# Kernel optimization log

Hardware: AMD Instinct MI355X
Metric: run time of the kernel (lower is better)

Reference implementation:

```python
import jax, jax.numpy as jnp
import numpy as np


def setup_inputs() -> dict:
    key = jax.random.key(0)
    ks = jax.random.split(key, 8)
    H = 4096
    T = 2048
    s = 0.02  # keep gates out of saturation
    return {
        "start_tensor": jax.random.normal(ks[0], (400,), jnp.float32),
        "encoder_hidden": jax.random.normal(ks[1], (1, 1, H), jnp.float32) * 0.1,
        "W_ih": jax.random.normal(ks[2], (3 * H, 400), jnp.float32) * s,
        "W_hh": jax.random.normal(ks[3], (3 * H, H), jnp.float32) * s,
        "b_ih": jax.random.normal(ks[4], (3 * H,), jnp.float32) * s,
        "b_hh": jax.random.normal(ks[5], (3 * H,), jnp.float32) * s,
        "W_out": jax.random.normal(ks[6], (401, H), jnp.float32) * s,
        "b_out": jax.random.normal(ks[7], (401,), jnp.float32) * s,
        "max_length": 2048,
    }


def reference(start_tensor, encoder_hidden, W_ih, W_hh, b_ih, b_hh, W_out, b_out, max_length):
    H = W_hh.shape[1]
    # The original loop feeds relu(start_tensor) as input at EVERY step
    # (input is never reassigned), so the input-side gate pre-activations
    # are loop-invariant and can be precomputed.
    x = jax.nn.relu(start_tensor)                      # [400]
    gx = W_ih @ x + b_ih                               # [3H]
    gx_r, gx_z, gx_n = gx[:H], gx[H:2 * H], gx[2 * H:]

    def step(h, _):
        gh = W_hh @ h + b_hh                           # [3H]
        r = jax.nn.sigmoid(gx_r + gh[:H])
        z = jax.nn.sigmoid(gx_z + gh[H:2 * H])
        n = jnp.tanh(gx_n + r * gh[2 * H:])
        h_new = (1.0 - z) * n + z * h                  # PyTorch GRU update
        o = W_out @ h_new + b_out                      # [401]
        out = jnp.tanh(o[:400])                        # [400]
        stop = jax.nn.sigmoid(o[400:])                 # [1]
        return h_new, (out, stop)

    h0 = encoder_hidden.reshape(H)
    _, (outputs, stops) = jax.lax.scan(step, h0, None, length=max_length)
    # outputs: [T, 400], stops: [T, 1]. The torch code breaks early when
    # stop > 0.5 (data-dependent length); here we run all steps (jit-safe).
    return outputs, stops
```

## Files before the change

### kernel.cpp

```cpp
#include <hip/hip_runtime.h>
#include <math.h>

#define NBLOCKS 256
#define NTHREADS 512
#define WPB 8
#define HDIM 4096
#define NPAIR (HDIM/2)

typedef _Float16 f16x2  __attribute__((ext_vector_type(2)));
typedef _Float16 f16x16 __attribute__((ext_vector_type(16)));
typedef unsigned long long u64;

union UF { unsigned u; f16x2 h; };

__device__ __forceinline__ float dot2f(f16x2 a, f16x2 b, float c) {
  return __builtin_amdgcn_fdot2(a, b, c, false);
}
__device__ __forceinline__ float sigmoidf_(float x) {
  return 1.0f / (1.0f + __expf(-x));
}
__device__ __forceinline__ float tanhf_(float x) {
  float a = fabsf(x);
  float t = __expf(-2.0f * a);
  float r = (1.0f - t) / (1.0f + t);
  return copysignf(r, x);
}
__device__ __forceinline__ void st64(u64* p, u64 v) {
  __hip_atomic_store(p, v, __ATOMIC_RELAXED, __HIP_MEMORY_SCOPE_AGENT);
}
__device__ __forceinline__ u64 ld64(const u64* p) {
  return __hip_atomic_load(p, __ATOMIC_RELAXED, __HIP_MEMORY_SCOPE_AGENT);
}

#define LOAD_CHUNK(VAR, SRC, C) do {                                          \
  const float2* s_ = (const float2*)(SRC) + lane + 64 * ((C) * 8);            \
  float2 p0_ = s_[0];   float2 p1_ = s_[64];  float2 p2_ = s_[128];           \
  float2 p3_ = s_[192]; float2 p4_ = s_[256]; float2 p5_ = s_[320];           \
  float2 p6_ = s_[384]; float2 p7_ = s_[448];                                 \
  VAR = (f16x16){ (_Float16)p0_.x, (_Float16)p0_.y, (_Float16)p1_.x, (_Float16)p1_.y, \
                  (_Float16)p2_.x, (_Float16)p2_.y, (_Float16)p3_.x, (_Float16)p3_.y, \
                  (_Float16)p4_.x, (_Float16)p4_.y, (_Float16)p5_.x, (_Float16)p5_.y, \
                  (_Float16)p6_.x, (_Float16)p6_.y, (_Float16)p7_.x, (_Float16)p7_.y }; \
} while (0)

#define LOAD_ROW(K, GATE, IDX) do {                                           \
  const float* sr_ = W_hh + ((size_t)(GATE) * HDIM + (i0 + (IDX))) * HDIM;    \
  LOAD_CHUNK(w##K##_0, sr_, 0); LOAD_CHUNK(w##K##_1, sr_, 1);                 \
  LOAD_CHUNK(w##K##_2, sr_, 2); LOAD_CHUNK(w##K##_3, sr_, 3);                 \
} while (0)

#define PAIR(V, J) (__builtin_shufflevector((V), (V), 2 * (J), 2 * (J) + 1))

#define DOT8(K, C)                                                            \
  a##K = dot2f(PAIR(w##K##_##C, 0), hp0, a##K);                               \
  a##K = dot2f(PAIR(w##K##_##C, 1), hp1, a##K);                               \
  a##K = dot2f(PAIR(w##K##_##C, 2), hp2, a##K);                               \
  a##K = dot2f(PAIR(w##K##_##C, 3), hp3, a##K);                               \
  a##K = dot2f(PAIR(w##K##_##C, 4), hp4, a##K);                               \
  a##K = dot2f(PAIR(w##K##_##C, 5), hp5, a##K);                               \
  a##K = dot2f(PAIR(w##K##_##C, 6), hp6, a##K);                               \
  a##K = dot2f(PAIR(w##K##_##C, 7), hp7, a##K);

#define CHUNK_STEP(C) {                                                       \
  UF u0_, u1_, u2_, u3_, u4_, u5_, u6_, u7_;                                  \
  u0_.u = h_lds[lane + 64 * ((C) * 8 + 0)];                                   \
  u1_.u = h_lds[lane + 64 * ((C) * 8 + 1)];                                   \
  u2_.u = h_lds[lane + 64 * ((C) * 8 + 2)];                                   \
  u3_.u = h_lds[lane + 64 * ((C) * 8 + 3)];                                   \
  u4_.u = h_lds[lane + 64 * ((C) * 8 + 4)];                                   \
  u5_.u = h_lds[lane + 64 * ((C) * 8 + 5)];                                   \
  u6_.u = h_lds[lane + 64 * ((C) * 8 + 6)];                                   \
  u7_.u = h_lds[lane + 64 * ((C) * 8 + 7)];                                   \
  f16x2 hp0 = u0_.h, hp1 = u1_.h, hp2 = u2_.h, hp3 = u3_.h;                   \
  f16x2 hp4 = u4_.h, hp5 = u5_.h, hp6 = u6_.h, hp7 = u7_.h;                   \
  DOT8(0, C) DOT8(1, C) DOT8(2, C) DOT8(3, C) DOT8(4, C) DOT8(5, C)          \
}

#define GX_INIT(K, GATE, IDX) {                                               \
  const int row_ = (GATE) * HDIM + (i0 + (IDX));                              \
  const float* s_ = W_ih + (size_t)row_ * 400;                                \
  float acc_ = 0.0f;                                                          \
  for (int c = lane; c < 400; c += 64) acc_ += s_[c] * x_lds[c];              \
  _Pragma("unroll")                                                           \
  for (int o = 32; o; o >>= 1) acc_ += __shfl_xor(acc_, o, 64);               \
  acc_ += b_ih[row_];                                                         \
  if ((GATE) != 2) acc_ += b_hh[row_];                                        \
  gx##K = acc_;                                                               \
}

__global__ __attribute__((amdgpu_flat_work_group_size(NTHREADS, NTHREADS),
                          amdgpu_waves_per_eu(2, 2)))
void gru_persistent(const float* __restrict__ start,
                    const float* __restrict__ enc_h,
                    const float* __restrict__ W_ih,
                    const float* __restrict__ W_hh,
                    const float* __restrict__ b_ih,
                    const float* __restrict__ b_hh,
                    const float* __restrict__ W_out,
                    const float* __restrict__ b_out,
                    float* __restrict__ out,
                    u64* __restrict__ ws,
                    int T)
{
  __shared__ unsigned h_lds[NPAIR];
  __shared__ unsigned wout_lds[2][NPAIR];
  __shared__ float    x_lds[400];

  const int tid  = threadIdx.x;
  const int b    = blockIdx.x;
  const int wave = tid >> 6;
  const int lane = tid & 63;
  const int g    = b * WPB + wave;
  const int i0   = 2 * g;

  u64* buf0 = ws;
  u64* buf1 = ws + NPAIR;

  if (tid < 400) x_lds[tid] = fmaxf(start[tid], 0.0f);
  for (int s = 0; s < 2; ++s) {
    int row = 2 * b + s;
    if (row < 401) {
      for (int p = tid; p < NPAIR; p += NTHREADS) {
        float2 wv = *(const float2*)(W_out + (size_t)row * HDIM + 2 * p);
        UF u; u.h = (f16x2){(_Float16)wv.x, (_Float16)wv.y};
        wout_lds[s][p] = u.u;
      }
    }
  }
  __syncthreads();

  f16x16 w0_0, w0_1, w0_2, w0_3;
  f16x16 w1_0, w1_1, w1_2, w1_3;
  f16x16 w2_0, w2_1, w2_2, w2_3;
  f16x16 w3_0, w3_1, w3_2, w3_3;
  f16x16 w4_0, w4_1, w4_2, w4_3;
  f16x16 w5_0, w5_1, w5_2, w5_3;
  LOAD_ROW(0, 0, 0); LOAD_ROW(1, 0, 1);
  LOAD_ROW(2, 1, 0); LOAD_ROW(3, 1, 1);
  LOAD_ROW(4, 2, 0); LOAD_ROW(5, 2, 1);

  float gx0, gx1, gx2, gx3, gx4, gx5;
  GX_INIT(0, 0, 0); GX_INIT(1, 0, 1);
  GX_INIT(2, 1, 0); GX_INIT(3, 1, 1);
  GX_INIT(4, 2, 0); GX_INIT(5, 2, 1);
  const float bhn0 = b_hh[2 * HDIM + i0];
  const float bhn1 = b_hh[2 * HDIM + i0 + 1];

  float h0 = enc_h[i0], h1 = enc_h[i0 + 1];

  if (lane == 0) {
    UF u; u.h = (f16x2){(_Float16)h0, (_Float16)h1};
    st64(&buf0[g], ((u64)1 << 32) | (u64)u.u);
  }

  for (int t = 0; t < T; ++t) {
    u64* rd = (t & 1) ? buf1 : buf0;
    u64* wr = (t & 1) ? buf0 : buf1;
    const unsigned exp = (unsigned)(t + 1);

    {
      const int p0 = tid, p1 = tid + NTHREADS, p2 = tid + 2 * NTHREADS, p3 = tid + 3 * NTHREADS;
      u64 v0, v1, v2, v3;
      for (;;) {
        v0 = ld64(rd + p0); v1 = ld64(rd + p1);
        v2 = ld64(rd + p2); v3 = ld64(rd + p3);
        if ((unsigned)(v0 >> 32) == exp && (unsigned)(v1 >> 32) == exp &&
            (unsigned)(v2 >> 32) == exp && (unsigned)(v3 >> 32) == exp) break;
        __builtin_amdgcn_s_sleep(1);
      }
      h_lds[p0] = (unsigned)v0; h_lds[p1] = (unsigned)v1;
      h_lds[p2] = (unsigned)v2; h_lds[p3] = (unsigned)v3;
    }
    __syncthreads();

    float a0 = 0.f, a1 = 0.f, a2 = 0.f, a3 = 0.f, a4 = 0.f, a5 = 0.f;
    CHUNK_STEP(0); CHUNK_STEP(1); CHUNK_STEP(2); CHUNK_STEP(3);
    #pragma unroll
    for (int off = 32; off; off >>= 1) {
      a0 += __shfl_xor(a0, off, 64);
      a1 += __shfl_xor(a1, off, 64);
      a2 += __shfl_xor(a2, off, 64);
      a3 += __shfl_xor(a3, off, 64);
      a4 += __shfl_xor(a4, off, 64);
      a5 += __shfl_xor(a5, off, 64);
    }

    float r0 = sigmoidf_(gx0 + a0);
    float r1 = sigmoidf_(gx1 + a1);
    float z0 = sigmoidf_(gx2 + a2);
    float z1 = sigmoidf_(gx3 + a3);
    float n0 = tanhf_(gx4 + r0 * (a4 + bhn0));
    float n1 = tanhf_(gx5 + r1 * (a5 + bhn1));
    h0 = (1.0f - z0) * n0 + z0 * h0;
    h1 = (1.0f - z1) * n1 + z1 * h1;

    if (lane == 0) {
      UF u; u.h = (f16x2){(_Float16)h0, (_Float16)h1};
      st64(&wr[g], ((u64)(unsigned)(t + 2) << 32) | (u64)u.u);
    }

    if (t > 0 && wave < 2) {
      int row = 2 * b + wave;
      if (row < 401) {
        float acc = 0.0f;
        #pragma unroll
        for (int j = 0; j < 32; ++j) {
          int p = lane + 64 * j;
          UF a, hh; a.u = wout_lds[wave][p]; hh.u = h_lds[p];
          acc = dot2f(a.h, hh.h, acc);
        }
        #pragma unroll
        for (int off = 32; off; off >>= 1) acc += __shfl_xor(acc, off, 64);
        if (lane == 0) {
          acc += b_out[row];
          if (row < 400) out[(size_t)(t - 1) * 400 + row] = tanhf_(acc);
          else           out[(size_t)400 * T + (t - 1)]   = sigmoidf_(acc);
        }
      }
    }
    __syncthreads();
  }

  {
    u64* rd = (T & 1) ? buf1 : buf0;
    const unsigned exp = (unsigned)(T + 1);
    const int p0 = tid, p1 = tid + NTHREADS, p2 = tid + 2 * NTHREADS, p3 = tid + 3 * NTHREADS;
    u64 v0, v1, v2, v3;
    for (;;) {
      v0 = ld64(rd + p0); v1 = ld64(rd + p1);
      v2 = ld64(rd + p2); v3 = ld64(rd + p3);
      if ((unsigned)(v0 >> 32) == exp && (unsigned)(v1 >> 32) == exp &&
          (unsigned)(v2 >> 32) == exp && (unsigned)(v3 >> 32) == exp) break;
      __builtin_amdgcn_s_sleep(1);
    }
    h_lds[p0] = (unsigned)v0; h_lds[p1] = (unsigned)v1;
    h_lds[p2] = (unsigned)v2; h_lds[p3] = (unsigned)v3;
    __syncthreads();
    if (wave < 2) {
      int row = 2 * b + wave;
      if (row < 401) {
        float acc = 0.0f;
        #pragma unroll
        for (int j = 0; j < 32; ++j) {
          int p = lane + 64 * j;
          UF a, hh; a.u = wout_lds[wave][p]; hh.u = h_lds[p];
          acc = dot2f(a.h, hh.h, acc);
        }
        #pragma unroll
        for (int off = 32; off; off >>= 1) acc += __shfl_xor(acc, off, 64);
        if (lane == 0) {
          acc += b_out[row];
          if (row < 400) out[(size_t)(T - 1) * 400 + row] = tanhf_(acc);
          else           out[(size_t)400 * T + (T - 1)]   = sigmoidf_(acc);
        }
      }
    }
  }
}

extern "C" void kernel_launch(void* const* d_in, const int* in_sizes, int n_in,
                              void* d_out, int out_size, void* d_ws, size_t ws_size,
                              hipStream_t stream) {
  (void)in_sizes; (void)n_in; (void)ws_size;
  const float* start = (const float*)d_in[0];
  const float* enc_h = (const float*)d_in[1];
  const float* W_ih  = (const float*)d_in[2];
  const float* W_hh  = (const float*)d_in[3];
  const float* b_ih  = (const float*)d_in[4];
  const float* b_hh  = (const float*)d_in[5];
  const float* W_out = (const float*)d_in[6];
  const float* b_out = (const float*)d_in[7];
  float* out = (float*)d_out;
  u64* ws = (u64*)d_ws;

  int T = out_size / 401;

  gru_persistent<<<NBLOCKS, NTHREADS, 0, stream>>>(
      start, enc_h, W_ih, W_hh, b_ih, b_hh, W_out, b_out, out, ws, T);
}
```

Baseline: 8.258 ms.

## Double-buffer h in LDS to drop trailing barrier and poll slots incrementally

```diff
diff --git a/kernel.cpp b/kernel.cpp
--- a/kernel.cpp
+++ b/kernel.cpp
@@ -63,14 +63,14 @@
 
 #define CHUNK_STEP(C) {                                                       \
   UF u0_, u1_, u2_, u3_, u4_, u5_, u6_, u7_;                                  \
-  u0_.u = h_lds[lane + 64 * ((C) * 8 + 0)];                                   \
-  u1_.u = h_lds[lane + 64 * ((C) * 8 + 1)];                                   \
-  u2_.u = h_lds[lane + 64 * ((C) * 8 + 2)];                                   \
-  u3_.u = h_lds[lane + 64 * ((C) * 8 + 3)];                                   \
-  u4_.u = h_lds[lane + 64 * ((C) * 8 + 4)];                                   \
-  u5_.u = h_lds[lane + 64 * ((C) * 8 + 5)];                                   \
-  u6_.u = h_lds[lane + 64 * ((C) * 8 + 6)];                                   \
-  u7_.u = h_lds[lane + 64 * ((C) * 8 + 7)];                                   \
+  u0_.u = hb[lane + 64 * ((C) * 8 + 0)];                                      \
+  u1_.u = hb[lane + 64 * ((C) * 8 + 1)];                                      \
+  u2_.u = hb[lane + 64 * ((C) * 8 + 2)];                                      \
+  u3_.u = hb[lane + 64 * ((C) * 8 + 3)];                                      \
+  u4_.u = hb[lane + 64 * ((C) * 8 + 4)];                                      \
+  u5_.u = hb[lane + 64 * ((C) * 8 + 5)];                                      \
+  u6_.u = hb[lane + 64 * ((C) * 8 + 6)];                                      \
+  u7_.u = hb[lane + 64 * ((C) * 8 + 7)];                                      \
   f16x2 hp0 = u0_.h, hp1 = u1_.h, hp2 = u2_.h, hp3 = u3_.h;                   \
   f16x2 hp4 = u4_.h, hp5 = u5_.h, hp6 = u6_.h, hp7 = u7_.h;                   \
   DOT8(0, C) DOT8(1, C) DOT8(2, C) DOT8(3, C) DOT8(4, C) DOT8(5, C)          \
@@ -87,6 +87,26 @@
   if ((GATE) != 2) acc_ += b_hh[row_];                                        \
   gx##K = acc_;                                                               \
 }
+
+#define SPIN_FILL(RD, EXP, HB) do {                                           \
+  const int q0 = tid, q1 = tid + NTHREADS, q2 = tid + 2 * NTHREADS,           \
+            q3 = tid + 3 * NTHREADS;                                          \
+  bool d0 = false, d1 = false, d2 = false, d3 = false;                        \
+  for (;;) {                                                                  \
+    u64 v0 = 0, v1 = 0, v2 = 0, v3 = 0;                                       \
+    if (!d0) v0 = ld64((RD) + q0);                                            \
+    if (!d1) v1 = ld64((RD) + q1);                                            \
+    if (!d2) v2 = ld64((RD) + q2);                                            \
+    if (!d3) v3 = ld64((RD) + q3);                                            \
+    if (!d0 && (unsigned)(v0 >> 32) == (EXP)) { (HB)[q0] = (unsigned)v0; d0 = true; } \
+    if (!d1 && (unsigned)(v1 >> 32) == (EXP)) { (HB)[q1] = (unsigned)v1; d1 = true; } \
+    if (!d2 && (unsigned)(v2 >> 32) == (EXP)) { (HB)[q2] = (unsigned)v2; d2 = true; } \
+    if (!d3 && (unsigned)(v3 >> 32) == (EXP)) { (HB)[q3] = (unsigned)v3; d3 = true; } \
+    if (d0 & d1 & d2 & d3) break;                                             \
+    if (d0 | d1 | d2 | d3) __builtin_amdgcn_s_sleep(1);                       \
+    else                   __builtin_amdgcn_s_sleep(2);                       \
+  }                                                                           \
+} while (0)
 
 __global__ __attribute__((amdgpu_flat_work_group_size(NTHREADS, NTHREADS),
                           amdgpu_waves_per_eu(2, 2)))
@@ -102,7 +122,7 @@
                     u64* __restrict__ ws,
                     int T)
 {
-  __shared__ unsigned h_lds[NPAIR];
+  __shared__ unsigned h_lds[2][NPAIR];
   __shared__ unsigned wout_lds[2][NPAIR];
   __shared__ float    x_lds[400];
 
@@ -157,20 +177,9 @@
     u64* rd = (t & 1) ? buf1 : buf0;
     u64* wr = (t & 1) ? buf0 : buf1;
     const unsigned exp = (unsigned)(t + 1);
-
-    {
-      const int p0 = tid, p1 = tid + NTHREADS, p2 = tid + 2 * NTHREADS, p3 = tid + 3 * NTHREADS;
-      u64 v0, v1, v2, v3;
-      for (;;) {
-        v0 = ld64(rd + p0); v1 = ld64(rd + p1);
-        v2 = ld64(rd + p2); v3 = ld64(rd + p3);
-        if ((unsigned)(v0 >> 32) == exp && (unsigned)(v1 >> 32) == exp &&
-            (unsigned)(v2 >> 32) == exp && (unsigned)(v3 >> 32) == exp) break;
-        __builtin_amdgcn_s_sleep(1);
-      }
-      h_lds[p0] = (unsigned)v0; h_lds[p1] = (unsigned)v1;
-      h_lds[p2] = (unsigned)v2; h_lds[p3] = (unsigned)v3;
-    }
+    unsigned* hb = h_lds[t & 1];
+
+    SPIN_FILL(rd, exp, hb);
     __syncthreads();
 
     float a0 = 0.f, a1 = 0.f, a2 = 0.f, a3 = 0.f, a4 = 0.f, a5 = 0.f;
@@ -206,7 +215,7 @@
         #pragma unroll
         for (int j = 0; j < 32; ++j) {
           int p = lane + 64 * j;
-          UF a, hh; a.u = wout_lds[wave][p]; hh.u = h_lds[p];
+          UF a, hh; a.u = wout_lds[wave][p]; hh.u = hb[p];
           acc = dot2f(a.h, hh.h, acc);
         }
         #pragma unroll
@@ -218,23 +227,13 @@
         }
       }
     }
-    __syncthreads();
   }
 
   {
     u64* rd = (T & 1) ? buf1 : buf0;
     const unsigned exp = (unsigned)(T + 1);
-    const int p0 = tid, p1 = tid + NTHREADS, p2 = tid + 2 * NTHREADS, p3 = tid + 3 * NTHREADS;
-    u64 v0, v1, v2, v3;
-    for (;;) {
-      v0 = ld64(rd + p0); v1 = ld64(rd + p1);
-      v2 = ld64(rd + p2); v3 = ld64(rd + p3);
-      if ((unsigned)(v0 >> 32) == exp && (unsigned)(v1 >> 32) == exp &&
-          (unsigned)(v2 >> 32) == exp && (unsigned)(v3 >> 32) == exp) break;
-      __builtin_amdgcn_s_sleep(1);
-    }
-    h_lds[p0] = (unsigned)v0; h_lds[p1] = (unsigned)v1;
-    h_lds[p2] = (unsigned)v2; h_lds[p3] = (unsigned)v3;
+    unsigned* hb = h_lds[T & 1];
+    SPIN_FILL(rd, exp, hb);
     __syncthreads();
     if (wave < 2) {
       int row = 2 * b + wave;
@@ -243,7 +242,7 @@
         #pragma unroll
         for (int j = 0; j < 32; ++j) {
           int p = lane + 64 * j;
-          UF a, hh; a.u = wout_lds[wave][p]; hh.u = h_lds[p];
+          UF a, hh; a.u = wout_lds[wave][p]; hh.u = hb[p];
           acc = dot2f(a.h, hh.h, acc);
         }
         #pragma unroll
```

After: 12.40 ms. 50.2% more time.
